# Performance work log

Hardware: AMD Instinct MI355X
Metric: run time of the kernel (lower is better)

Reference implementation:

```python
import jax, jax.numpy as jnp
import numpy as np

MEM_SIZE = 2000
FEA_DIM = 256
FMAP = 32
BATCH = 32
SHRINK = 0.0025
EPS = 1e-12


def setup_inputs() -> dict:
    key = jax.random.key(0)
    k1, k2, k3, k4 = jax.random.split(key, 4)
    stdv = 1.0 / np.sqrt(FEA_DIM)
    inp = {
        "input": jax.random.normal(k1, (BATCH, FEA_DIM, FMAP, FMAP), dtype=jnp.float32),
        "label_batch": jax.random.randint(k2, (BATCH,), 0, 2),
        "weight": jax.random.uniform(k3, (MEM_SIZE, FEA_DIM), dtype=jnp.float32, minval=-stdv, maxval=stdv),
        "pos_embedding": jax.random.normal(k4, (1, FEA_DIM, FMAP, FMAP), dtype=jnp.float32),
    }
    return inp


def _forward(x, weight, pos_embedding):
    b, c, h, w = x.shape
    m = weight.shape[0]
    x = x + pos_embedding  # pos=True
    xr = x.transpose(0, 2, 3, 1).reshape(-1, c)  # [b*h*w, c]
    # addressing: linear -> softmax over memory slots
    att = jax.nn.softmax(jnp.einsum('nc,mc->nm', xr, weight), axis=1)  # [N, m]
    # compact loss: MSE to nearest memory item (argmax of att before shrink)
    idx = jnp.argmax(att, axis=1)
    pos_item = weight[idx]  # [N, c]
    compact_loss = jnp.mean((xr - pos_item) ** 2)
    # distance loss: hinge on pairwise squared distances between memory items
    sq = jnp.sum(weight * weight, axis=1)
    d2 = sq[:, None] + sq[None, :] - 2.0 * (weight @ weight.T)  # [m, m]
    dist = 1.0 - d2
    dist = dist * (dist > 0).astype(dist.dtype)
    dist = jnp.triu(dist, k=1)
    distance_loss = dist.sum() * 2.0 / (m * (m - 1))
    # hard shrink relu + L1 normalize (shrink_thres > 0)
    att = jax.nn.relu(att - SHRINK) * att / (jnp.abs(att - SHRINK) + EPS)
    att = att / jnp.maximum(jnp.sum(jnp.abs(att), axis=1, keepdims=True), EPS)
    # memory read
    out = jnp.einsum('nm,mc->nc', att, weight)
    out = out.reshape(b, h, w, c).transpose(0, 3, 1, 2)
    return out, compact_loss, distance_loss


def reference(input, label_batch, weight, pos_embedding):
    return _forward(input, weight, pos_embedding)
```

## Files before the change

### kernel.cpp

```cpp
#include <hip/hip_runtime.h>
#include <hip/hip_bf16.h>

typedef unsigned char u8;
typedef unsigned short u16;
typedef unsigned int u32;
typedef long long s64;
typedef float f32x4 __attribute__((ext_vector_type(4)));

#define MEM    2000
#define FEA    256
#define SLSTR  2056
#define OSTR   265
#define XRS    264
#define RING   65792
#define POOLSZ 131328
#define OUTN   8388608

typedef const __attribute__((address_space(1))) u32* gp1;
typedef __attribute__((address_space(3))) u32* lp3;

__device__ __forceinline__ void gl_lds16(const void* g, void* l) {
    __builtin_amdgcn_global_load_lds((gp1)g, (lp3)l, 16, 0, 0);
}
__device__ __forceinline__ void pipe_bar() {
    __builtin_amdgcn_sched_barrier(0);
    __builtin_amdgcn_s_barrier();
    __builtin_amdgcn_sched_barrier(0);
}
__device__ __forceinline__ void lds_bar() {
    asm volatile("s_waitcnt lgkmcnt(0)" ::: "memory");
    pipe_bar();
}

__device__ __forceinline__ u32 f2e4m3(float x) {
    float ax = fabsf(x);
    u32 s = (__builtin_bit_cast(u32, x) >> 24) & 0x80u;
    if (ax >= 448.f) return s | 0x7e;
    if (ax < 0.015625f) {
        int q = (int)rintf(ax * 512.f);
        return s | (u32)q;
    }
    int e = (int)(__builtin_bit_cast(u32, ax) >> 23) - 127;
    float scale = __builtin_bit_cast(float, (u32)((127 - e + 3) << 23));
    int q = (int)rintf(ax * scale);
    int E = e + 7;
    if (q == 16) { q = 8; E += 1; if (E > 15) return s | 0x7e; }
    return s | (u32)(E << 3) | (u32)(q & 7);
}
__device__ __forceinline__ u32 f2e4m3_fast(float v) {
    u32 u = __builtin_bit_cast(u32, v);
    u += 0x0007FFFFu + ((u >> 20) & 1u);
    int bb = (int)(u >> 20) - 0x3C0;
    return bb < 0 ? 0u : (u32)bb;
}

__global__ __launch_bounds__(256) void prep_kernel(const float* __restrict__ W,
                                                   u8* __restrict__ WTc,
                                                   u8* __restrict__ Wc,
                                                   float* __restrict__ sqv,
                                                   float* __restrict__ loss) {
    const int blk = blockIdx.x, t = threadIdx.x;
    const int m0 = blk * 8;
    {
        const int sl = t >> 5, cl = t & 31;
        const int slot = m0 + sl;
        const int ch0 = cl * 8;
        const float* wr = W + slot * 256 + ch0;
        f32x4 v0 = *(const f32x4*)wr;
        f32x4 v1 = *(const f32x4*)(wr + 4);
        float ss = v0[0]*v0[0] + v0[1]*v0[1] + v0[2]*v0[2] + v0[3]*v0[3]
                 + v1[0]*v1[0] + v1[1]*v1[1] + v1[2]*v1[2] + v1[3]*v1[3];
        ss += __shfl_xor(ss, 1); ss += __shfl_xor(ss, 2); ss += __shfl_xor(ss, 4);
        ss += __shfl_xor(ss, 8); ss += __shfl_xor(ss, 16);
        if (cl == 0) sqv[slot] = ss;
        const int c = slot >> 6, s = slot & 63;
        const int kk = cl >> 2, agp = cl & 3;
        u32 lo = 0, hi = 0;
#pragma unroll
        for (int i = 0; i < 4; ++i) {
            lo |= f2e4m3(v0[i] * 16.f) << (i * 8);
            hi |= f2e4m3(v1[i] * 16.f) << (i * 8);
        }
        u8* dst = Wc + c * 16384 + (size_t)((kk * 4 + agp) * 64 + s) * 8;
        *(u32*)dst = lo;
        *(u32*)(dst + 4) = hi;
    }
    {
        const int ch = t;
        const int chunk = m0 >> 6, kl0 = m0 & 63;
        u32 lo = 0, hi = 0;
#pragma unroll
        for (int i = 0; i < 8; ++i) {
            u32 bb = f2e4m3(W[(m0 + i) * 256 + ch] * 16.f);
            if (i < 4) lo |= bb << (i * 8); else hi |= bb << ((i - 4) * 8);
        }
        u8* dst = WTc + chunk * 16384 + ch * 64 + (kl0 ^ ((ch & 7) << 3));
        *(u32*)dst = lo;
        *(u32*)(dst + 4) = hi;
    }
    if (blk == 0 && t == 0) {
        loss[0] = 0.0f;
        loss[1] = -2000.0f / (2000.0f * 1999.0f);
    }
}

__global__ __launch_bounds__(512, 1) void main_kernel(
        const float* __restrict__ inp, const float* __restrict__ posb,
        const u8* __restrict__ Wc, const u8* __restrict__ WTc,
        const float* __restrict__ sqv, float* __restrict__ out,
        float* __restrict__ loss) {
    __shared__ __align__(16) u8 pool[POOLSZ];
    __shared__ float sPM[4][32];
    __shared__ int   sPI[4][32];
    __shared__ float sPZ[4][32];
    __shared__ float sPD[4][32];
    __shared__ float sSS[8][32];
    __shared__ float sMax[32];
    __shared__ float sThr[32];
    __shared__ float sInv[32];

    const int t = threadIdx.x;
    const int w = t >> 6, lane = t & 63;
    const int ar = lane & 15, ag = lane >> 4;
    const int blk = blockIdx.x, b = blk >> 5, hw0 = (blk & 31) << 5;
    const int prot = ((blk >> 3) & 15) * 2;
    const int q = w & 3, rt = w >> 2;
    const int row_a = rt * 16 + ar;

#pragma unroll
    for (int u = 0; u < 2; ++u) {
        const int pc = (u + prot) & 31;
        const u8* src = Wc + pc * 16384 + w * 2048 + lane * 16;
        u8* dst = pool + RING + u * 16384 + w * 2048;
        gl_lds16(src, dst);
        gl_lds16(src + 1024, dst + 1024);
    }

    {
        const int hw = t & 31, cg = t >> 5;
        const float* ip = inp + (size_t)b * 262144 + hw0 + hw;
        const float* pp = posb + hw0 + hw;
        float ss = 0.f;
        u8* xrow = pool + hw * XRS + cg * 16;
#pragma unroll
        for (int j = 0; j < 8; ++j) {
            const int ch = cg * 16 + 2 * j;
            float v0 = ip[ch * 1024] + pp[ch * 1024];
            float v1 = ip[(ch + 1) * 1024] + pp[(ch + 1) * 1024];
            ss += v0 * v0 + v1 * v1;
            u16 pk2 = (u16)(f2e4m3(v0 * 4.f) | (f2e4m3(v1 * 4.f) << 8));
            *(u16*)(xrow + 2 * j) = pk2;
        }
        ss += __shfl_xor(ss, 32);
        if (lane < 32) sSS[w][lane] = ss;
    }
    lds_bar();

    s64 xB[8];
#pragma unroll
    for (int kk = 0; kk < 8; ++kk)
        xB[kk] = *(const s64*)(pool + row_a * XRS + kk * 32 + ag * 8);
    asm volatile("s_waitcnt lgkmcnt(0)" ::: "memory");
    __builtin_amdgcn_sched_barrier(0);

    f32x4 acc[32];
    const int c31 = (31 - prot) & 31;
#pragma unroll
    for (int i = 0; i < 16; ++i) {
        asm volatile("s_waitcnt vmcnt(0)" ::: "memory");
        pipe_bar();
        if (i < 15) {
#pragma unroll
            for (int u = 0; u < 2; ++u) {
                const int cl = 2 * i + 2 + u;
                const int pc = (cl + prot) & 31;
                const u8* src = Wc + pc * 16384 + w * 2048 + lane * 16;
                u8* dst = pool + RING + (cl & 3) * 16384 + w * 2048;
                gl_lds16(src, dst);
                gl_lds16(src + 1024, dst + 1024);
            }
        }
#pragma unroll
        for (int u = 0; u < 2; ++u) {
            const int cl = 2 * i + u;
            const u8* base = pool + RING + (cl & 3) * 16384;
            f32x4 a = {0.f, 0.f, 0.f, 0.f};
#pragma unroll
            for (int kk = 0; kk < 8; ++kk) {
                s64 wA = *(const s64*)(base + ((kk * 4 + ag) * 64 + q * 16 + ar) * 8);
                a = __builtin_amdgcn_mfma_f32_16x16x32_fp8_fp8(wA, xB[kk], a, 0, 0, 0);
            }
            if (cl == c31 && q != 0) { a[0] = -3e38f; a[1] = -3e38f; a[2] = -3e38f; a[3] = -3e38f; }
            acc[cl] = a;
        }
    }

    {
        float bm = -3e38f; int bi = 0x7fffffff;
#pragma unroll
        for (int c = 0; c < 32; ++c) {
            const int cb = (((c + prot) & 31) << 6) + q * 16 + ag * 4;
#pragma unroll
            for (int e = 0; e < 4; ++e) {
                float f = acc[c][e];
                int id = cb + e;
                if (f > bm || (f == bm && id < bi)) { bm = f; bi = id; }
            }
        }
#pragma unroll
        for (int d = 16; d < 64; d <<= 1) {
            float om = __shfl_xor(bm, d);
            int   oi = __shfl_xor(bi, d);
            if (om > bm || (om == bm && oi < bi)) { bm = om; bi = oi; }
        }
        if (lane < 16) { sPM[q][rt * 16 + lane] = bm; sPI[q][rt * 16 + lane] = bi; }
    }

#pragma unroll
    for (int u = 0; u < 2; ++u) {
        const int pc = (u + prot) & 31;
        const u8* src = WTc + pc * 16384 + w * 2048 + lane * 16;
        u8* dst = pool + RING + u * 16384 + w * 2048;
        gl_lds16(src, dst);
        gl_lds16(src + 1024, dst + 1024);
    }
    lds_bar();

    if (t < 32) {
        float mx = sPM[0][t]; int bid = sPI[0][t];
#pragma unroll
        for (int qq = 1; qq < 4; ++qq) {
            float m2 = sPM[qq][t]; int i2 = sPI[qq][t];
            if (m2 > mx || (m2 == mx && i2 < bid)) { mx = m2; bid = i2; }
        }
        sMax[t] = mx;
        float ssq = 0.f;
#pragma unroll
        for (int ww = 0; ww < 8; ++ww) ssq += sSS[ww][t];
        float term = ssq - 2.f * (mx * 0.015625f) + sqv[bid];
#pragma unroll
        for (int d = 1; d < 32; d <<= 1) term += __shfl_xor(term, d);
        if (t == 0) atomicAdd(loss, term * (1.0f / 8388608.0f));
    }
    lds_bar();

    {
        const float mxv = sMax[row_a];
        float z = 0.f;
#pragma unroll
        for (int c = 0; c < 32; ++c)
#pragma unroll
            for (int e = 0; e < 4; ++e) {
                float a_ = __expf((acc[c][e] - mxv) * 0.015625f);
                acc[c][e] = a_;
                z += a_;
            }
        z += __shfl_xor(z, 16); z += __shfl_xor(z, 32);
        if (lane < 16) sPZ[q][rt * 16 + lane] = z;
    }
    lds_bar();
    if (t < 32) sThr[t] = 0.0025f * (sPZ[0][t] + sPZ[1][t] + sPZ[2][t] + sPZ[3][t]);
    lds_bar();

    {
        const float thrv = sThr[row_a];
        const int rowbase = row_a * SLSTR + q * 16 + ag * 4;
        float den = 0.f;
#pragma unroll
        for (int c = 0; c < 32; ++c) {
            const int off = rowbase + (((c + prot) & 31) << 6);
            u32 pk = 0;
#pragma unroll
            for (int e = 0; e < 4; ++e) {
                float a_ = acc[c][e];
                if (a_ > thrv) { den += a_; pk |= f2e4m3_fast(a_ * 64.f) << (e * 8); }
            }
            *(u32*)(pool + off) = pk;
        }
        den += __shfl_xor(den, 16); den += __shfl_xor(den, 32);
        if (lane < 16) sPD[q][rt * 16 + lane] = den;
    }
    lds_bar();
    if (t < 32) {
        float dd = sPD[0][t] + sPD[1][t] + sPD[2][t] + sPD[3][t];
        sInv[t] = dd > 0.f ? 1.0f / (1024.0f * dd) : 0.0f;
    }
    lds_bar();

    const int ch0 = (w * 2) * 16 + ar;
    const int ch1 = ch0 + 16;
    int bo[2][2];
#pragma unroll
    for (int kk = 0; kk < 2; ++kk) {
        bo[0][kk] = (ch0 * 64 + kk * 32 + ag * 8) ^ ((ch0 & 7) << 3);
        bo[1][kk] = (ch1 * 64 + kk * 32 + ag * 8) ^ ((ch1 & 7) << 3);
    }
    const u8* sLr0 = pool + ar * SLSTR + ag * 8;
    const u8* sLr1 = pool + (16 + ar) * SLSTR + ag * 8;
    f32x4 o00 = {0.f,0.f,0.f,0.f}, o01 = {0.f,0.f,0.f,0.f};
    f32x4 o10 = {0.f,0.f,0.f,0.f}, o11 = {0.f,0.f,0.f,0.f};
#pragma unroll
    for (int i = 0; i < 16; ++i) {
        asm volatile("s_waitcnt vmcnt(0)" ::: "memory");
        pipe_bar();
        if (i < 15) {
#pragma unroll
            for (int u = 0; u < 2; ++u) {
                const int cl = 2 * i + 2 + u;
                const int pc = (cl + prot) & 31;
                const u8* src = WTc + pc * 16384 + w * 2048 + lane * 16;
                u8* dst = pool + RING + (cl & 3) * 16384 + w * 2048;
                gl_lds16(src, dst);
                gl_lds16(src + 1024, dst + 1024);
            }
        }
#pragma unroll
        for (int u = 0; u < 2; ++u) {
            const int cl = 2 * i + u;
            const u8* base = pool + RING + (cl & 3) * 16384;
            const int cc64 = ((cl + prot) & 31) << 6;
            s64 A00 = *(const s64*)(sLr0 + cc64);
            s64 A01 = *(const s64*)(sLr0 + cc64 + 32);
            s64 A10 = *(const s64*)(sLr1 + cc64);
            s64 A11 = *(const s64*)(sLr1 + cc64 + 32);
            s64 B00 = *(const s64*)(base + bo[0][0]);
            s64 B01 = *(const s64*)(base + bo[0][1]);
            s64 B10 = *(const s64*)(base + bo[1][0]);
            s64 B11 = *(const s64*)(base + bo[1][1]);
            o00 = __builtin_amdgcn_mfma_f32_16x16x32_fp8_fp8(A00, B00, o00, 0, 0, 0);
            o00 = __builtin_amdgcn_mfma_f32_16x16x32_fp8_fp8(A01, B01, o00, 0, 0, 0);
            o01 = __builtin_amdgcn_mfma_f32_16x16x32_fp8_fp8(A10, B00, o01, 0, 0, 0);
            o01 = __builtin_amdgcn_mfma_f32_16x16x32_fp8_fp8(A11, B01, o01, 0, 0, 0);
            o10 = __builtin_amdgcn_mfma_f32_16x16x32_fp8_fp8(A00, B10, o10, 0, 0, 0);
            o10 = __builtin_amdgcn_mfma_f32_16x16x32_fp8_fp8(A01, B11, o10, 0, 0, 0);
            o11 = __builtin_amdgcn_mfma_f32_16x16x32_fp8_fp8(A10, B10, o11, 0, 0, 0);
            o11 = __builtin_amdgcn_mfma_f32_16x16x32_fp8_fp8(A11, B11, o11, 0, 0, 0);
        }
    }
    lds_bar();

    {
        float* sO = (float*)pool;
#pragma unroll
        for (int i = 0; i < 4; ++i) {
            int r0 = ag * 4 + i, r1 = 16 + ag * 4 + i;
            sO[r0 * OSTR + ch0] = o00[i] * sInv[r0];
            sO[r1 * OSTR + ch0] = o01[i] * sInv[r1];
            sO[r0 * OSTR + ch1] = o10[i] * sInv[r0];
            sO[r1 * OSTR + ch1] = o11[i] * sInv[r1];
        }
    }
    lds_bar();
    {
        const float* sO = (const float*)pool;
        const int hw = t & 31, cq = t >> 5;
        float* op = out + (size_t)b * 262144 + hw0 + hw;
#pragma unroll
        for (int i = 0; i < 16; ++i) {
            int ch = cq + (i << 4);
            op[ch * 1024] = sO[hw * OSTR + ch];
        }
    }
}

__global__ __launch_bounds__(256) void dist_kernel(const u8* __restrict__ Wc,
                                                   const float* __restrict__ sqv,
                                                   float* __restrict__ dl) {
    __shared__ float red[4];
    int t = threadIdx.x, w = t >> 6, lane = t & 63;
    int ar = lane & 15, ag = lane >> 4;
    const int i0 = blockIdx.x << 4;
    const int ci = i0 >> 6, si0 = i0 & 63;
    s64 af8[8];
#pragma unroll
    for (int kk = 0; kk < 8; ++kk)
        af8[kk] = *(const s64*)(Wc + ci * 16384 + (size_t)((kk * 4 + ag) * 64 + si0 + ar) * 8);
    float sqi[4];
#pragma unroll
    for (int e = 0; e < 4; ++e) sqi[e] = sqv[i0 + ag * 4 + e];
    float sum = 0.f;
    for (int jt = w; jt < 125; jt += 4) {
        const int j0 = jt << 4;
        const int cj = j0 >> 6, sj0 = j0 & 63;
        f32x4 acc = {0.f, 0.f, 0.f, 0.f};
#pragma unroll
        for (int kk = 0; kk < 8; ++kk) {
            s64 bf = *(const s64*)(Wc + cj * 16384 + (size_t)((kk * 4 + ag) * 64 + sj0 + ar) * 8);
            acc = __builtin_amdgcn_mfma_f32_16x16x32_fp8_fp8(af8[kk], bf, acc, 0, 0, 0);
        }
        float sqj = sqv[j0 + ar];
#pragma unroll
        for (int e = 0; e < 4; ++e) {
            float dist = 1.0f - (sqi[e] + sqj - acc[e] * 0.0078125f);
            sum += dist > 0.f ? dist : 0.f;
        }
    }
#pragma unroll
    for (int d = 1; d < 64; d <<= 1) sum += __shfl_xor(sum, d);
    if (lane == 0) red[w] = sum;
    __syncthreads();
    if (t == 0) {
        float s = red[0] + red[1] + red[2] + red[3];
        atomicAdd(dl, s * (1.0f / (2000.0f * 1999.0f)));
    }
}

extern "C" void kernel_launch(void* const* d_in, const int* in_sizes, int n_in,
                              void* d_out, int out_size, void* d_ws, size_t ws_size,
                              hipStream_t stream) {
    (void)in_sizes; (void)n_in; (void)out_size; (void)ws_size;
    const float* inp  = (const float*)d_in[0];
    const float* W    = (const float*)d_in[2];
    const float* posb = (const float*)d_in[3];
    float* out = (float*)d_out;

    u8* WTc = (u8*)d_ws;
    u8* Wc  = (u8*)d_ws + 524288;
    float* sqv = (float*)((u8*)d_ws + 1048576);

    hipLaunchKernelGGL(prep_kernel, dim3(250), dim3(256), 0, stream, W, WTc, Wc, sqv, out + OUTN);
    hipLaunchKernelGGL(main_kernel, dim3(1024), dim3(512), 0, stream, inp, posb, Wc, WTc, sqv, out, out + OUTN);
    hipLaunchKernelGGL(dist_kernel, dim3(125), dim3(256), 0, stream, Wc, sqv, out + OUTN + 1);
}
```

Measured before the change: 180.8 us.

## Pair fp8 K-slices for 128-bit LDS reads and deepen first GEMM ring

Repacks the fp8 weight layout so two adjacent K-slices sit contiguously, letting the first GEMM, the distance kernel and the memory-read A operand use 128-bit loads instead of pairs of 64-bit loads. The first GEMM's weight ring grows to six buffers with a prefetch distance of four chunks and a partial vmcnt wait, separate from a dedicated ring for the transposed weights. The attention staging layout and its stride change to match the wider reads. The aim is fewer LDS instructions and better hiding of global-to-LDS latency, at the cost of a larger LDS footprint that may reduce occupancy.

```diff
diff --git a/kernel.cpp b/kernel.cpp
--- a/kernel.cpp
+++ b/kernel.cpp
@@ -6,14 +6,16 @@
 typedef unsigned int u32;
 typedef long long s64;
 typedef float f32x4 __attribute__((ext_vector_type(4)));
+typedef long long s64x2 __attribute__((ext_vector_type(2)));
 
 #define MEM    2000
 #define FEA    256
-#define SLSTR  2056
+#define SLSTR  2064
 #define OSTR   265
 #define XRS    264
-#define RING   65792
-#define POOLSZ 131328
+#define XRBASE 98304
+#define RING2  66048
+#define POOLSZ 131584
 #define OUTN   8388608
 
 typedef const __attribute__((address_space(1))) u32* gp1;
@@ -75,13 +77,14 @@
         if (cl == 0) sqv[slot] = ss;
         const int c = slot >> 6, s = slot & 63;
         const int kk = cl >> 2, agp = cl & 3;
+        const int kp = kk >> 1, klo = kk & 1;
         u32 lo = 0, hi = 0;
 #pragma unroll
         for (int i = 0; i < 4; ++i) {
             lo |= f2e4m3(v0[i] * 16.f) << (i * 8);
             hi |= f2e4m3(v1[i] * 16.f) << (i * 8);
         }
-        u8* dst = Wc + c * 16384 + (size_t)((kk * 4 + agp) * 64 + s) * 8;
+        u8* dst = Wc + c * 16384 + (size_t)((kp * 4 + agp) * 64 + s) * 16 + klo * 8;
         *(u32*)dst = lo;
         *(u32*)(dst + 4) = hi;
     }
@@ -128,10 +131,10 @@
     const int row_a = rt * 16 + ar;
 
 #pragma unroll
-    for (int u = 0; u < 2; ++u) {
-        const int pc = (u + prot) & 31;
+    for (int cl = 0; cl < 4; ++cl) {
+        const int pc = (cl + prot) & 31;
         const u8* src = Wc + pc * 16384 + w * 2048 + lane * 16;
-        u8* dst = pool + RING + u * 16384 + w * 2048;
+        u8* dst = pool + (cl % 6) * 16384 + w * 2048;
         gl_lds16(src, dst);
         gl_lds16(src + 1024, dst + 1024);
     }
@@ -141,7 +144,7 @@
         const float* ip = inp + (size_t)b * 262144 + hw0 + hw;
         const float* pp = posb + hw0 + hw;
         float ss = 0.f;
-        u8* xrow = pool + hw * XRS + cg * 16;
+        u8* xrow = pool + XRBASE + hw * XRS + cg * 16;
 #pragma unroll
         for (int j = 0; j < 8; ++j) {
             const int ch = cg * 16 + 2 * j;
@@ -159,12 +162,152 @@
     s64 xB[8];
 #pragma unroll
     for (int kk = 0; kk < 8; ++kk)
-        xB[kk] = *(const s64*)(pool + row_a * XRS + kk * 32 + ag * 8);
+        xB[kk] = *(const s64*)(pool + XRBASE + row_a * XRS + kk * 32 + ag * 8);
     asm volatile("s_waitcnt lgkmcnt(0)" ::: "memory");
     __builtin_amdgcn_sched_barrier(0);
 
     f32x4 acc[32];
     const int c31 = (31 - prot) & 31;
+    {
+        const int rowoff = (q * 16 + ar) * 16;
+#pragma unroll
+        for (int i = 0; i < 16; ++i) {
+            if (i <= 14) asm volatile("s_waitcnt vmcnt(4)" ::: "memory");
+            else         asm volatile("s_waitcnt vmcnt(0)" ::: "memory");
+            pipe_bar();
+            if (i <= 13) {
+#pragma unroll
+                for (int u = 0; u < 2; ++u) {
+                    const int cl = 2 * i + 4 + u;
+                    const int pc = (cl + prot) & 31;
+                    const u8* src = Wc + pc * 16384 + w * 2048 + lane * 16;
+                    u8* dst = pool + (cl % 6) * 16384 + w * 2048;
+                    gl_lds16(src, dst);
+                    gl_lds16(src + 1024, dst + 1024);
+                }
+            }
+#pragma unroll
+            for (int u = 0; u < 2; ++u) {
+                const int cl = 2 * i + u;
+                const u8* base = pool + (cl % 6) * 16384 + rowoff;
+                f32x4 a = {0.f, 0.f, 0.f, 0.f};
+#pragma unroll
+                for (int kp = 0; kp < 4; ++kp) {
+                    s64x2 wA = *(const s64x2*)(base + (kp * 4 + ag) * 1024);
+                    a = __builtin_amdgcn_mfma_f32_16x16x32_fp8_fp8(wA[0], xB[2 * kp], a, 0, 0, 0);
+                    a = __builtin_amdgcn_mfma_f32_16x16x32_fp8_fp8(wA[1], xB[2 * kp + 1], a, 0, 0, 0);
+                }
+                if (cl == c31 && q != 0) { a[0] = -3e38f; a[1] = -3e38f; a[2] = -3e38f; a[3] = -3e38f; }
+                acc[cl] = a;
+            }
+        }
+    }
+
+    {
+        float bm = -3e38f; int bi = 0x7fffffff;
+#pragma unroll
+        for (int c = 0; c < 32; ++c) {
+            const int cb = (((c + prot) & 31) << 6) + q * 16 + ag * 4;
+#pragma unroll
+            for (int e = 0; e < 4; ++e) {
+                float f = acc[c][e];
+                int id = cb + e;
+                if (f > bm || (f == bm && id < bi)) { bm = f; bi = id; }
+            }
+        }
+#pragma unroll
+        for (int d = 16; d < 64; d <<= 1) {
+            float om = __shfl_xor(bm, d);
+            int   oi = __shfl_xor(bi, d);
+            if (om > bm || (om == bm && oi < bi)) { bm = om; bi = oi; }
+        }
+        if (lane < 16) { sPM[q][rt * 16 + lane] = bm; sPI[q][rt * 16 + lane] = bi; }
+    }
+
+#pragma unroll
+    for (int u = 0; u < 2; ++u) {
+        const int pc = (u + prot) & 31;
+        const u8* src = WTc + pc * 16384 + w * 2048 + lane * 16;
+        u8* dst = pool + RING2 + u * 16384 + w * 2048;
+        gl_lds16(src, dst);
+        gl_lds16(src + 1024, dst + 1024);
+    }
+    lds_bar();
+
+    if (t < 32) {
+        float mx = sPM[0][t]; int bid = sPI[0][t];
+#pragma unroll
+        for (int qq = 1; qq < 4; ++qq) {
+            float m2 = sPM[qq][t]; int i2 = sPI[qq][t];
+            if (m2 > mx || (m2 == mx && i2 < bid)) { mx = m2; bid = i2; }
+        }
+        sMax[t] = mx;
+        float ssq = 0.f;
+#pragma unroll
+        for (int ww = 0; ww < 8; ++ww) ssq += sSS[ww][t];
+        float term = ssq - 2.f * (mx * 0.015625f) + sqv[bid];
+#pragma unroll
+        for (int d = 1; d < 32; d <<= 1) term += __shfl_xor(term, d);
+        if (t == 0) atomicAdd(loss, term * (1.0f / 8388608.0f));
+    }
+    lds_bar();
+
+    {
+        const float mxv = sMax[row_a];
+        float z = 0.f;
+#pragma unroll
+        for (int c = 0; c < 32; ++c)
+#pragma unroll
+            for (int e = 0; e < 4; ++e) {
+                float a_ = __expf((acc[c][e] - mxv) * 0.015625f);
+                acc[c][e] = a_;
+                z += a_;
+            }
+        z += __shfl_xor(z, 16); z += __shfl_xor(z, 32);
+        if (lane < 16) sPZ[q][rt * 16 + lane] = z;
+    }
+    lds_bar();
+    if (t < 32) sThr[t] = 0.0025f * (sPZ[0][t] + sPZ[1][t] + sPZ[2][t] + sPZ[3][t]);
+    lds_bar();
+
+    {
+        const float thrv = sThr[row_a];
+        const int newoff = (((q * 2 + (ag >> 1)) & 3) << 4) | ((q >> 1) << 3) | ((ag & 1) << 2);
+        const int rowbase = row_a * SLSTR + newoff;
+        float den = 0.f;
+#pragma unroll
+        for (int c = 0; c < 32; ++c) {
+            const int off = rowbase + (((c + prot) & 31) << 6);
+            u32 pk = 0;
+#pragma unroll
+            for (int e = 0; e < 4; ++e) {
+                float a_ = acc[c][e];
+                if (a_ > thrv) { den += a_; pk |= f2e4m3_fast(a_ * 64.f) << (e * 8); }
+            }
+            *(u32*)(pool + off) = pk;
+        }
+        den += __shfl_xor(den, 16); den += __shfl_xor(den, 32);
+        if (lane < 16) sPD[q][rt * 16 + lane] = den;
+    }
+    lds_bar();
+    if (t < 32) {
+        float dd = sPD[0][t] + sPD[1][t] + sPD[2][t] + sPD[3][t];
+        sInv[t] = dd > 0.f ? 1.0f / (1024.0f * dd) : 0.0f;
+    }
+    lds_bar();
+
+    const int ch0 = (w * 2) * 16 + ar;
+    const int ch1 = ch0 + 16;
+    int bo[2][2];
+#pragma unroll
+    for (int kk = 0; kk < 2; ++kk) {
+        bo[0][kk] = (ch0 * 64 + kk * 32 + ag * 8) ^ ((ch0 & 7) << 3);
+        bo[1][kk] = (ch1 * 64 + kk * 32 + ag * 8) ^ ((ch1 & 7) << 3);
+    }
+    const u8* sLr0 = pool + ar * SLSTR + ag * 16;
+    const u8* sLr1 = pool + (16 + ar) * SLSTR + ag * 16;
+    f32x4 o00 = {0.f,0.f,0.f,0.f}, o01 = {0.f,0.f,0.f,0.f};
+    f32x4 o10 = {0.f,0.f,0.f,0.f}, o11 = {0.f,0.f,0.f,0.f};
 #pragma unroll
     for (int i = 0; i < 16; ++i) {
         asm volatile("s_waitcnt vmcnt(0)" ::: "memory");
@@ -174,8 +317,8 @@
             for (int u = 0; u < 2; ++u) {
                 const int cl = 2 * i + 2 + u;
                 const int pc = (cl + prot) & 31;
-                const u8* src = Wc + pc * 16384 + w * 2048 + lane * 16;
-                u8* dst = pool + RING + (cl & 3) * 16384 + w * 2048;
+                const u8* src = WTc + pc * 16384 + w * 2048 + lane * 16;
+                u8* dst = pool + RING2 + (cl & 3) * 16384 + w * 2048;
                 gl_lds16(src, dst);
                 gl_lds16(src + 1024, dst + 1024);
             }
@@ -183,158 +326,22 @@
 #pragma unroll
         for (int u = 0; u < 2; ++u) {
             const int cl = 2 * i + u;
-            const u8* base = pool + RING + (cl & 3) * 16384;
-            f32x4 a = {0.f, 0.f, 0.f, 0.f};
-#pragma unroll
-            for (int kk = 0; kk < 8; ++kk) {
-                s64 wA = *(const s64*)(base + ((kk * 4 + ag) * 64 + q * 16 + ar) * 8);
-                a = __builtin_amdgcn_mfma_f32_16x16x32_fp8_fp8(wA, xB[kk], a, 0, 0, 0);
-            }
-            if (cl == c31 && q != 0) { a[0] = -3e38f; a[1] = -3e38f; a[2] = -3e38f; a[3] = -3e38f; }
-            acc[cl] = a;
-        }
-    }
-
-    {
-        float bm = -3e38f; int bi = 0x7fffffff;
-#pragma unroll
-        for (int c = 0; c < 32; ++c) {
-            const int cb = (((c + prot) & 31) << 6) + q * 16 + ag * 4;
-#pragma unroll
-            for (int e = 0; e < 4; ++e) {
-                float f = acc[c][e];
-                int id = cb + e;
-                if (f > bm || (f == bm && id < bi)) { bm = f; bi = id; }
-            }
-        }
-#pragma unroll
-        for (int d = 16; d < 64; d <<= 1) {
-            float om = __shfl_xor(bm, d);
-            int   oi = __shfl_xor(bi, d);
-            if (om > bm || (om == bm && oi < bi)) { bm = om; bi = oi; }
-        }
-        if (lane < 16) { sPM[q][rt * 16 + lane] = bm; sPI[q][rt * 16 + lane] = bi; }
-    }
-
-#pragma unroll
-    for (int u = 0; u < 2; ++u) {
-        const int pc = (u + prot) & 31;
-        const u8* src = WTc + pc * 16384 + w * 2048 + lane * 16;
-        u8* dst = pool + RING + u * 16384 + w * 2048;
-        gl_lds16(src, dst);
-        gl_lds16(src + 1024, dst + 1024);
-    }
-    lds_bar();
-
-    if (t < 32) {
-        float mx = sPM[0][t]; int bid = sPI[0][t];
-#pragma unroll
-        for (int qq = 1; qq < 4; ++qq) {
-            float m2 = sPM[qq][t]; int i2 = sPI[qq][t];
-            if (m2 > mx || (m2 == mx && i2 < bid)) { mx = m2; bid = i2; }
-        }
-        sMax[t] = mx;
-        float ssq = 0.f;
-#pragma unroll
-        for (int ww = 0; ww < 8; ++ww) ssq += sSS[ww][t];
-        float term = ssq - 2.f * (mx * 0.015625f) + sqv[bid];
-#pragma unroll
-        for (int d = 1; d < 32; d <<= 1) term += __shfl_xor(term, d);
-        if (t == 0) atomicAdd(loss, term * (1.0f / 8388608.0f));
-    }
-    lds_bar();
-
-    {
-        const float mxv = sMax[row_a];
-        float z = 0.f;
-#pragma unroll
-        for (int c = 0; c < 32; ++c)
-#pragma unroll
-            for (int e = 0; e < 4; ++e) {
-                float a_ = __expf((acc[c][e] - mxv) * 0.015625f);
-                acc[c][e] = a_;
-                z += a_;
-            }
-        z += __shfl_xor(z, 16); z += __shfl_xor(z, 32);
-        if (lane < 16) sPZ[q][rt * 16 + lane] = z;
-    }
-    lds_bar();
-    if (t < 32) sThr[t] = 0.0025f * (sPZ[0][t] + sPZ[1][t] + sPZ[2][t] + sPZ[3][t]);
-    lds_bar();
-
-    {
-        const float thrv = sThr[row_a];
-        const int rowbase = row_a * SLSTR + q * 16 + ag * 4;
-        float den = 0.f;
-#pragma unroll
-        for (int c = 0; c < 32; ++c) {
-            const int off = rowbase + (((c + prot) & 31) << 6);
-            u32 pk = 0;
-#pragma unroll
-            for (int e = 0; e < 4; ++e) {
-                float a_ = acc[c][e];
-                if (a_ > thrv) { den += a_; pk |= f2e4m3_fast(a_ * 64.f) << (e * 8); }
-            }
-            *(u32*)(pool + off) = pk;
-        }
-        den += __shfl_xor(den, 16); den += __shfl_xor(den, 32);
-        if (lane < 16) sPD[q][rt * 16 + lane] = den;
-    }
-    lds_bar();
-    if (t < 32) {
-        float dd = sPD[0][t] + sPD[1][t] + sPD[2][t] + sPD[3][t];
-        sInv[t] = dd > 0.f ? 1.0f / (1024.0f * dd) : 0.0f;
-    }
-    lds_bar();
-
-    const int ch0 = (w * 2) * 16 + ar;
-    const int ch1 = ch0 + 16;
-    int bo[2][2];
-#pragma unroll
-    for (int kk = 0; kk < 2; ++kk) {
-        bo[0][kk] = (ch0 * 64 + kk * 32 + ag * 8) ^ ((ch0 & 7) << 3);
-        bo[1][kk] = (ch1 * 64 + kk * 32 + ag * 8) ^ ((ch1 & 7) << 3);
-    }
-    const u8* sLr0 = pool + ar * SLSTR + ag * 8;
-    const u8* sLr1 = pool + (16 + ar) * SLSTR + ag * 8;
-    f32x4 o00 = {0.f,0.f,0.f,0.f}, o01 = {0.f,0.f,0.f,0.f};
-    f32x4 o10 = {0.f,0.f,0.f,0.f}, o11 = {0.f,0.f,0.f,0.f};
-#pragma unroll
-    for (int i = 0; i < 16; ++i) {
-        asm volatile("s_waitcnt vmcnt(0)" ::: "memory");
-        pipe_bar();
-        if (i < 15) {
-#pragma unroll
-            for (int u = 0; u < 2; ++u) {
-                const int cl = 2 * i + 2 + u;
-                const int pc = (cl + prot) & 31;
-                const u8* src = WTc + pc * 16384 + w * 2048 + lane * 16;
-                u8* dst = pool + RING + (cl & 3) * 16384 + w * 2048;
-                gl_lds16(src, dst);
-                gl_lds16(src + 1024, dst + 1024);
-            }
-        }
-#pragma unroll
-        for (int u = 0; u < 2; ++u) {
-            const int cl = 2 * i + u;
-            const u8* base = pool + RING + (cl & 3) * 16384;
+            const u8* base = pool + RING2 + (cl & 3) * 16384;
             const int cc64 = ((cl + prot) & 31) << 6;
-            s64 A00 = *(const s64*)(sLr0 + cc64);
-            s64 A01 = *(const s64*)(sLr0 + cc64 + 32);
-            s64 A10 = *(const s64*)(sLr1 + cc64);
-            s64 A11 = *(const s64*)(sLr1 + cc64 + 32);
+            s64x2 A0 = *(const s64x2*)(sLr0 + cc64);
+            s64x2 A1 = *(const s64x2*)(sLr1 + cc64);
             s64 B00 = *(const s64*)(base + bo[0][0]);
             s64 B01 = *(const s64*)(base + bo[0][1]);
             s64 B10 = *(const s64*)(base + bo[1][0]);
             s64 B11 = *(const s64*)(base + bo[1][1]);
-            o00 = __builtin_amdgcn_mfma_f32_16x16x32_fp8_fp8(A00, B00, o00, 0, 0, 0);
-            o00 = __builtin_amdgcn_mfma_f32_16x16x32_fp8_fp8(A01, B01, o00, 0, 0, 0);
-            o01 = __builtin_amdgcn_mfma_f32_16x16x32_fp8_fp8(A10, B00, o01, 0, 0, 0);
-            o01 = __builtin_amdgcn_mfma_f32_16x16x32_fp8_fp8(A11, B01, o01, 0, 0, 0);
-            o10 = __builtin_amdgcn_mfma_f32_16x16x32_fp8_fp8(A00, B10, o10, 0, 0, 0);
-            o10 = __builtin_amdgcn_mfma_f32_16x16x32_fp8_fp8(A01, B11, o10, 0, 0, 0);
-            o11 = __builtin_amdgcn_mfma_f32_16x16x32_fp8_fp8(A10, B10, o11, 0, 0, 0);
-            o11 = __builtin_amdgcn_mfma_f32_16x16x32_fp8_fp8(A11, B11, o11, 0, 0, 0);
+            o00 = __builtin_amdgcn_mfma_f32_16x16x32_fp8_fp8(A0[0], B00, o00, 0, 0, 0);
+            o00 = __builtin_amdgcn_mfma_f32_16x16x32_fp8_fp8(A0[1], B01, o00, 0, 0, 0);
+            o01 = __builtin_amdgcn_mfma_f32_16x16x32_fp8_fp8(A1[0], B00, o01, 0, 0, 0);
+            o01 = __builtin_amdgcn_mfma_f32_16x16x32_fp8_fp8(A1[1], B01, o01, 0, 0, 0);
+            o10 = __builtin_amdgcn_mfma_f32_16x16x32_fp8_fp8(A0[0], B10, o10, 0, 0, 0);
+            o10 = __builtin_amdgcn_mfma_f32_16x16x32_fp8_fp8(A0[1], B11, o10, 0, 0, 0);
+            o11 = __builtin_amdgcn_mfma_f32_16x16x32_fp8_fp8(A1[0], B10, o11, 0, 0, 0);
+            o11 = __builtin_amdgcn_mfma_f32_16x16x32_fp8_fp8(A1[1], B11, o11, 0, 0, 0);
         }
     }
     lds_bar();
@@ -371,10 +378,10 @@
     int ar = lane & 15, ag = lane >> 4;
     const int i0 = blockIdx.x << 4;
     const int ci = i0 >> 6, si0 = i0 & 63;
-    s64 af8[8];
-#pragma unroll
-    for (int kk = 0; kk < 8; ++kk)
-        af8[kk] = *(const s64*)(Wc + ci * 16384 + (size_t)((kk * 4 + ag) * 64 + si0 + ar) * 8);
+    s64x2 af2[4];
+#pragma unroll
+    for (int kp = 0; kp < 4; ++kp)
+        af2[kp] = *(const s64x2*)(Wc + ci * 16384 + (size_t)((kp * 4 + ag) * 64 + si0 + ar) * 16);
     float sqi[4];
 #pragma unroll
     for (int e = 0; e < 4; ++e) sqi[e] = sqv[i0 + ag * 4 + e];
@@ -384,9 +391,10 @@
         const int cj = j0 >> 6, sj0 = j0 & 63;
         f32x4 acc = {0.f, 0.f, 0.f, 0.f};
 #pragma unroll
-        for (int kk = 0; kk < 8; ++kk) {
-            s64 bf = *(const s64*)(Wc + cj * 16384 + (size_t)((kk * 4 + ag) * 64 + sj0 + ar) * 8);
-            acc = __builtin_amdgcn_mfma_f32_16x16x32_fp8_fp8(af8[kk], bf, acc, 0, 0, 0);
+        for (int kp = 0; kp < 4; ++kp) {
+            s64x2 bf = *(const s64x2*)(Wc + cj * 16384 + (size_t)((kp * 4 + ag) * 64 + sj0 + ar) * 16);
+            acc = __builtin_amdgcn_mfma_f32_16x16x32_fp8_fp8(af2[kp][0], bf[0], acc, 0, 0, 0);
+            acc = __builtin_amdgcn_mfma_f32_16x16x32_fp8_fp8(af2[kp][1], bf[1], acc, 0, 0, 0);
         }
         float sqj = sqv[j0 + ar];
 #pragma unroll
```

Result: faster. 174.3 us (-3.6%).
